# Kernel tuning notes

Measured on AMD Instinct MI355X. Metric: run time of the kernel, lower is better.

Reference implementation:

```python
import jax, jax.numpy as jnp
import numpy as np

N = 100000
IN_C = 128
HID = 8
HEADS = 8
OUT_C = 16
NEG_SLOPE = 0.2  # PyG GATConv default leaky_relu slope
EPS = 1e-16


def setup_inputs() -> dict:
    key = jax.random.key(0)
    ks = jax.random.split(key, 10)
    E = 1600000
    x = jax.random.normal(ks[0], (N, IN_C), dtype=jnp.float32)
    edge_index = jax.random.randint(ks[1], (2, E), 0, N, dtype=jnp.int64)
    g = lambda k, shape: jax.random.normal(k, shape, dtype=jnp.float32) * 0.1
    # layer 1: in -> hid, heads=HEADS, concat
    W1 = g(ks[2], (IN_C, HEADS * HID))
    att_src1 = g(ks[3], (HEADS, HID))
    att_dst1 = g(ks[4], (HEADS, HID))
    b1 = jnp.zeros((HEADS * HID,), jnp.float32)
    # layer 2: hid*heads -> out, heads=1, concat=False (mean)
    W2 = g(ks[5], (HEADS * HID, 1 * OUT_C))
    att_src2 = g(ks[6], (1, OUT_C))
    att_dst2 = g(ks[7], (1, OUT_C))
    b2 = jnp.zeros((OUT_C,), jnp.float32)
    return {"x": x, "edge_index": edge_index, "W1": W1, "att_src1": att_src1,
            "att_dst1": att_dst1, "b1": b1, "W2": W2, "att_src2": att_src2,
            "att_dst2": att_dst2, "b2": b2}


def gat_conv(x, src, dst, W, att_src, att_dst, bias, concat):
    # x: [N, F_in]; src/dst: [E] (self-loops already included)
    H, C = att_src.shape
    h = (x @ W).reshape(N, H, C)                      # [N, H, C]
    a_src = jnp.sum(h * att_src, axis=-1)             # [N, H]
    a_dst = jnp.sum(h * att_dst, axis=-1)             # [N, H]
    alpha = a_src[src] + a_dst[dst]                   # [E, H]
    alpha = jax.nn.leaky_relu(alpha, NEG_SLOPE)
    # segment softmax over incoming edges of each destination node
    amax = jax.ops.segment_max(alpha, dst, num_segments=N)
    alpha = jnp.exp(alpha - amax[dst])
    asum = jax.ops.segment_sum(alpha, dst, num_segments=N)
    alpha = alpha / (asum[dst] + EPS)                 # [E, H]
    # (attention dropout skipped: eval mode)
    out = jax.ops.segment_sum(h[src] * alpha[:, :, None], dst, num_segments=N)  # [N, H, C]
    out = out.reshape(N, H * C) if concat else out.mean(axis=1)
    return out + bias


def reference(x, edge_index, W1, att_src1, att_dst1, b1, W2, att_src2, att_dst2, b2):
    # PyG GATConv adds self-loops by default
    loop = jnp.arange(N, dtype=edge_index.dtype)
    src = jnp.concatenate([edge_index[0], loop])
    dst = jnp.concatenate([edge_index[1], loop])
    h = gat_conv(x, src, dst, W1, att_src1, att_dst1, b1, concat=True)
    h = jax.nn.relu(h)
    out = gat_conv(h, src, dst, W2, att_src2, att_dst2, b2, concat=False)
    return jax.nn.relu(out)
```

## Files before the change

kernel.cpp:

```cpp
#include <hip/hip_runtime.h>
#include <hip/hip_fp16.h>

#define IN_C 128
#define NEG 0.2f
#define GAT_EPS 1e-16f
#define B_N 128
#define NB_MAX 1024
#define TILE 2048
#define GEMM_BLKS 782
#define CAP 2560
#define CS_STRIDE 72

typedef _Float16 half8 __attribute__((ext_vector_type(8)));
typedef float f32x4 __attribute__((ext_vector_type(4)));

static __device__ inline unsigned f2h(float f) {
    _Float16 h = (_Float16)f;
    unsigned short u;
    __builtin_memcpy(&u, &h, 2);
    return (unsigned)u;
}

__global__ __launch_bounds__(256) void k2_kernel(
    const float* __restrict__ x, const float* __restrict__ W1,
    const float* __restrict__ att_s1, const float* __restrict__ att_d1,
    float* __restrict__ hp, __half* __restrict__ a_src1, float* __restrict__ a_dst1,
    const int* __restrict__ ei, int* __restrict__ bucketCnt, unsigned* __restrict__ ebuf,
    int E, int Etot, int NB, int N, int egrid)
{
    __shared__ __align__(16) char smem[26112];
    int tid = threadIdx.x;

    if ((int)blockIdx.x < egrid) {
        int* lcnt  = (int*)smem;
        int* lbase = lcnt + NB_MAX;
        for (int i = tid; i < NB; i += 256) lcnt[i] = 0;
        __syncthreads();
        int base = (int)blockIdx.x * TILE;
        for (int k = tid; k < TILE; k += 256) {
            int e = base + k;
            if (e < Etot) {
                int dst = (e < E) ? ei[E + e] : (e - E);
                atomicAdd(&lcnt[dst >> 7], 1);
            }
        }
        __syncthreads();
        for (int i = tid; i < NB; i += 256) {
            int c = lcnt[i];
            lbase[i] = c ? (i * CAP + atomicAdd(&bucketCnt[i], c)) : 0;
        }
        __syncthreads();
        for (int i = tid; i < NB; i += 256) lcnt[i] = 0;
        __syncthreads();
        for (int k = tid; k < TILE; k += 256) {
            int e = base + k;
            if (e < Etot) {
                int src, dst;
                if (e < E) { src = ei[e]; dst = ei[E + e]; }
                else       { src = dst = e - E; }
                int b = dst >> 7;
                int r = atomicAdd(&lcnt[b], 1);
                int pos = lbase[b] + r;
                if (pos < (b + 1) * CAP)
                    ebuf[pos] = ((unsigned)(dst & (B_N - 1)) << 25) | (unsigned)src;
            }
        }
        return;
    }

    _Float16* bfrag = (_Float16*)smem;
    _Float16* csbase = (_Float16*)(smem + 16384);
    float* attS = (float*)(smem + 16384 + 9216);
    float* attD = attS + 64;
    if (tid < 64) { attS[tid] = att_s1[tid]; attD[tid] = att_d1[tid]; }
    for (int idx = tid; idx < 8192; idx += 256) {
        int f = idx >> 9;
        int l = (idx >> 3) & 63;
        int j = idx & 7;
        int k0 = f >> 2, nt = f & 3;
        int row = k0 * 32 + ((l >> 4) << 3) + j;
        int col = (nt << 4) + (l & 15);
        bfrag[idx] = (_Float16)W1[row * 64 + col];
    }
    __syncthreads();

    int lane = tid & 63, wid = tid >> 6;
    _Float16* csw = csbase + wid * (16 * CS_STRIDE);
    int mrow = lane & 15;
    int kgrp = lane >> 4;
    const half8* bf8 = (const half8*)bfrag;
    int ntiles = (N + 15) >> 4;
    int gb = (int)blockIdx.x - egrid;
    for (int t0 = (gb << 3) + (wid << 1); t0 < ntiles; t0 += (GEMM_BLKS << 3)) {
        bool has1 = (t0 + 1) < ntiles;
        int n0 = t0 << 4;
        int arow0 = n0 + mrow;        if (arow0 >= N) arow0 = N - 1;
        int arow1 = n0 + 16 + mrow;   if (arow1 >= N) arow1 = N - 1;
        const float* xr0 = x + (size_t)arow0 * IN_C + (kgrp << 3);
        const float* xr1 = x + (size_t)arow1 * IN_C + (kgrp << 3);
        f32x4 accs[2][4] = {};
        #pragma unroll
        for (int k0 = 0; k0 < 4; ++k0) {
            float4 xa0 = *(const float4*)(xr0 + k0 * 32);
            float4 xb0 = *(const float4*)(xr0 + k0 * 32 + 4);
            float4 xa1 = *(const float4*)(xr1 + k0 * 32);
            float4 xb1 = *(const float4*)(xr1 + k0 * 32 + 4);
            half8 a0, a1;
            a0[0] = (_Float16)xa0.x; a0[1] = (_Float16)xa0.y;
            a0[2] = (_Float16)xa0.z; a0[3] = (_Float16)xa0.w;
            a0[4] = (_Float16)xb0.x; a0[5] = (_Float16)xb0.y;
            a0[6] = (_Float16)xb0.z; a0[7] = (_Float16)xb0.w;
            a1[0] = (_Float16)xa1.x; a1[1] = (_Float16)xa1.y;
            a1[2] = (_Float16)xa1.z; a1[3] = (_Float16)xa1.w;
            a1[4] = (_Float16)xb1.x; a1[5] = (_Float16)xb1.y;
            a1[6] = (_Float16)xb1.z; a1[7] = (_Float16)xb1.w;
            #pragma unroll
            for (int nt = 0; nt < 4; ++nt) {
                accs[0][nt] = __builtin_amdgcn_mfma_f32_16x16x32_f16(a0, bf8[(k0 * 4 + nt) * 64 + lane], accs[0][nt], 0, 0, 0);
                accs[1][nt] = __builtin_amdgcn_mfma_f32_16x16x32_f16(a1, bf8[(k0 * 4 + nt) * 64 + lane], accs[1][nt], 0, 0, 0);
            }
        }
        #pragma unroll
        for (int tt = 0; tt < 2; ++tt) {
            if (tt == 1 && !has1) break;
            int nb0 = n0 + (tt << 4);
            #pragma unroll
            for (int r = 0; r < 4; ++r) {
                int row = (kgrp << 2) + r;
                csw[row * CS_STRIDE +  0 + mrow] = (_Float16)accs[tt][0][r];
                csw[row * CS_STRIDE + 16 + mrow] = (_Float16)accs[tt][1][r];
                csw[row * CS_STRIDE + 32 + mrow] = (_Float16)accs[tt][2][r];
                csw[row * CS_STRIDE + 48 + mrow] = (_Float16)accs[tt][3][r];
            }
            asm volatile("s_waitcnt lgkmcnt(0)" ::: "memory");
            {
                int node = lane >> 2, cq = lane & 3;
                int n = nb0 + node;
                if (n < N) {
                    const int4* src = (const int4*)(csw + node * CS_STRIDE + (cq << 4));
                    int4 v0 = src[0];
                    int4 v1 = src[1];
                    char* dst = (char*)(hp + (size_t)n * 32) + (cq << 5);
                    ((int4*)dst)[0] = v0;
                    ((int4*)dst)[1] = v1;
                }
            }
            #pragma unroll
            for (int pr = 0; pr < 2; ++pr) {
                int node = (pr << 3) + (lane >> 3), head = lane & 7;
                int n = nb0 + node;
                if (n < N) {
                    const half8* hv = (const half8*)(csw + node * CS_STRIDE + (head << 3));
                    half8 v = *hv;
                    float s = 0.f, d = 0.f;
                    #pragma unroll
                    for (int c = 0; c < 8; ++c) {
                        float vv = (float)v[c];
                        s = fmaf(vv, attS[(head << 3) + c], s);
                        d = fmaf(vv, attD[(head << 3) + c], d);
                    }
                    a_src1[n * 8 + head] = __float2half(s);
                    a_dst1[n * 8 + head] = d;
                }
            }
        }
    }
}

__global__ __launch_bounds__(256) void bucket_sort_kernel(
    const unsigned* __restrict__ ebuf, const int* __restrict__ bucketCnt,
    int2* __restrict__ rowse, int* __restrict__ esrc, int N)
{
    __shared__ int lhist[B_N];
    __shared__ int lstart[B_N];
    __shared__ int wsum1;
    int blk = blockIdx.x, t = threadIdx.x;
    int e0 = blk * CAP;
    int cnt = bucketCnt[blk]; if (cnt > CAP) cnt = CAP;
    int e1 = e0 + cnt;
    if (t < B_N) lhist[t] = 0;
    __syncthreads();
    for (int k = e0 + t; k < e1; k += 256)
        atomicAdd(&lhist[ebuf[k] >> 25], 1);
    __syncthreads();
    int lane = t & 63;
    if (t < B_N) {
        int s = lhist[t];
        for (int off = 1; off < 64; off <<= 1) {
            int u = __shfl_up(s, off);
            if (lane >= off) s += u;
        }
        lstart[t] = s;
        if (t == 63) wsum1 = s;
    }
    __syncthreads();
    if (t < B_N) {
        int s = lstart[t];
        if (t >= 64) s += wsum1;
        int excl = s - lhist[t];
        lstart[t] = excl;
        int n = blk * B_N + t;
        if (n < N) rowse[n] = make_int2(e0 + excl, e0 + excl + lhist[t]);
    }
    __syncthreads();
    if (t < B_N) lhist[t] = 0;
    __syncthreads();
    for (int k = e0 + t; k < e1; k += 256) {
        unsigned pk = ebuf[k];
        int d = pk >> 25;
        int r = atomicAdd(&lhist[d], 1);
        esrc[e0 + lstart[d] + r] = (int)(pk & 0x1FFFFFF);
    }
}

__global__ __launch_bounds__(256) void agg1g2_kernel(
    const int* __restrict__ esrc, const int2* __restrict__ rowse,
    const float* __restrict__ hp, const __half* __restrict__ a_src1,
    const float* __restrict__ a_dst1, const float* __restrict__ b1,
    const float* __restrict__ W2, const float* __restrict__ att_s2,
    const float* __restrict__ att_d2, __half* __restrict__ h2w,
    float* __restrict__ a_src2, float* __restrict__ a_dst2, int N)
{
    __shared__ _Float16 w2frag[1024];
    __shared__ _Float16 h2s[4][16][64];
    __shared__ float cs[4][16 * 20];
    int tid = threadIdx.x;
    for (int idx = tid; idx < 1024; idx += 256) {
        int f = idx >> 9, l = (idx >> 3) & 63, j = idx & 7;
        int row = f * 32 + ((l >> 4) << 3) + j;
        int col = l & 15;
        w2frag[idx] = (_Float16)W2[row * 16 + col];
    }
    __syncthreads();

    int lane = tid & 63, wid = tid >> 6;
    int half = lane >> 5, c2 = lane & 31;
    int h = c2 >> 2;
    int ch = c2 & 7;
    int sbase = half * 32 + h;
    float2 bb = *(const float2*)(b1 + 2 * c2);
    int mrow = lane & 15, kgrp = lane >> 4;
    const half8* w2bf8 = (const half8*)w2frag;
    float* csw = &cs[wid][0];
    int ech = (lane & 3) << 2;
    float as0 = att_s2[ech], as1 = att_s2[ech + 1], as2 = att_s2[ech + 2], as3 = att_s2[ech + 3];
    float ad0 = att_d2[ech], ad1 = att_d2[ech + 1], ad2 = att_d2[ech + 2], ad3 = att_d2[ech + 3];

    int ngroups = (N + 63) >> 6;
    for (int grp = blockIdx.x; grp < ngroups; grp += gridDim.x) {
        int wbase = (grp << 6) + (wid << 4);
        for (int sub = 0; sub < 8; ++sub) {
            int nloc = (sub << 1) + half;
            int n = wbase + nloc;
            bool act = (n < N);
            int nn = act ? n : 0;
            int2 se = rowse[nn];
            int p = se.x;
            int end = act ? se.y : se.x;
            float ad_f = a_dst1[nn * 8 + h];
            float ad_c = a_dst1[nn * 8 + ch];
            float ax = 0.f, ay = 0.f, wsum = 0.f;
            for (; p + 3 < end; p += 4) {
                int s0 = esrc[p], s1 = esrc[p + 1], s2 = esrc[p + 2], s3 = esrc[p + 3];
                int se_ = (c2 & 16) ? ((c2 & 8) ? s3 : s2) : ((c2 & 8) ? s1 : s0);
                float ac = __half2float(a_src1[se_ * 8 + ch]) + ad_c;
                ac = (ac > 0.f) ? ac : NEG * ac;
                float wl = __expf(ac);
                float w0 = __shfl(wl, sbase);
                float w1 = __shfl(wl, sbase + 8);
                float w2 = __shfl(wl, sbase + 16);
                float w3 = __shfl(wl, sbase + 24);
                __half2 q0 = ((const __half2*)(hp + (size_t)s0 * 32))[c2];
                __half2 q1 = ((const __half2*)(hp + (size_t)s1 * 32))[c2];
                __half2 q2 = ((const __half2*)(hp + (size_t)s2 * 32))[c2];
                __half2 q3 = ((const __half2*)(hp + (size_t)s3 * 32))[c2];
                ax = fmaf(w0, __low2float(q0), ax);  ay = fmaf(w0, __high2float(q0), ay);
                ax = fmaf(w1, __low2float(q1), ax);  ay = fmaf(w1, __high2float(q1), ay);
                ax = fmaf(w2, __low2float(q2), ax);  ay = fmaf(w2, __high2float(q2), ay);
                ax = fmaf(w3, __low2float(q3), ax);  ay = fmaf(w3, __high2float(q3), ay);
                wsum += (w0 + w1) + (w2 + w3);
            }
            for (; p < end; ++p) {
                int s0 = esrc[p];
                float a0 = __half2float(a_src1[s0 * 8 + h]) + ad_f;
                __half2 q0 = ((const __half2*)(hp + (size_t)s0 * 32))[c2];
                a0 = (a0 > 0.f) ? a0 : NEG * a0;
                float w0 = __expf(a0);
                ax = fmaf(w0, __low2float(q0), ax);
                ay = fmaf(w0, __high2float(q0), ay);
                wsum += w0;
            }
            float inv = 1.f / (wsum + GAT_EPS);
            float vx = fmaf(ax, inv, bb.x);
            float vy = fmaf(ay, inv, bb.y);
            vx = (act && vx > 0.f) ? vx : 0.f;
            vy = (act && vy > 0.f) ? vy : 0.f;
            ((__half2*)&h2s[wid][nloc][0])[c2] =
                __halves2half2(__float2half(vx), __float2half(vy));
        }
        asm volatile("s_waitcnt lgkmcnt(0)" ::: "memory");
        f32x4 acc = {0, 0, 0, 0};
        const half8* ar = (const half8*)&h2s[wid][mrow][0];
        acc = __builtin_amdgcn_mfma_f32_16x16x32_f16(ar[kgrp], w2bf8[lane], acc, 0, 0, 0);
        acc = __builtin_amdgcn_mfma_f32_16x16x32_f16(ar[4 + kgrp], w2bf8[64 + lane], acc, 0, 0, 0);
        #pragma unroll
        for (int r = 0; r < 4; ++r)
            csw[((kgrp << 2) + r) * 20 + mrow] = acc[r];
        asm volatile("s_waitcnt lgkmcnt(0)" ::: "memory");
        int node = lane >> 2;
        int n = wbase + node;
        if (n < N) {
            float4 v = *(const float4*)&csw[node * 20 + ech];
            unsigned pk0 = f2h(v.x) | (f2h(v.y) << 16);
            unsigned pk1 = f2h(v.z) | (f2h(v.w) << 16);
            *(int2*)((char*)(h2w + (size_t)n * 16) + (ech << 1)) = make_int2((int)pk0, (int)pk1);
            float s = fmaf(v.x, as0, fmaf(v.y, as1, fmaf(v.z, as2, v.w * as3)));
            float d = fmaf(v.x, ad0, fmaf(v.y, ad1, fmaf(v.z, ad2, v.w * ad3)));
            s += __shfl_xor(s, 1); d += __shfl_xor(d, 1);
            s += __shfl_xor(s, 2); d += __shfl_xor(d, 2);
            if ((lane & 3) == 0) { a_src2[n] = s; a_dst2[n] = d; }
        }
    }
}

__global__ __launch_bounds__(256) void agg2_kernel(
    const int* __restrict__ esrc, const int2* __restrict__ rowse,
    const __half* __restrict__ h2w, const float* __restrict__ a_src2,
    const float* __restrict__ a_dst2, const float* __restrict__ b2,
    float* __restrict__ out, int N)
{
    int wslot = (blockIdx.x * 256 + threadIdx.x) >> 6;
    int nw = (gridDim.x * 256) >> 6;
    int lane = threadIdx.x & 63;
    int oct = lane >> 3, c2 = lane & 7;
    for (int base = wslot * 8; base < N; base += nw * 8) {
        int n = base + oct;
        bool act = (n < N);
        int nn = act ? n : 0;
        int2 se = rowse[nn];
        int p = se.x;
        int end = act ? se.y : se.x;
        float ad = a_dst2[nn];
        float ax = 0.f, ay = 0.f, wsum = 0.f;
        for (; p + 3 < end; p += 4) {
            int s0 = esrc[p], s1 = esrc[p + 1], s2 = esrc[p + 2], s3 = esrc[p + 3];
            float a0 = a_src2[s0] + ad;
            float a1 = a_src2[s1] + ad;
            float a2 = a_src2[s2] + ad;
            float a3 = a_src2[s3] + ad;
            __half2 q0 = ((const __half2*)(h2w + (size_t)s0 * 16))[c2];
            __half2 q1 = ((const __half2*)(h2w + (size_t)s1 * 16))[c2];
            __half2 q2 = ((const __half2*)(h2w + (size_t)s2 * 16))[c2];
            __half2 q3 = ((const __half2*)(h2w + (size_t)s3 * 16))[c2];
            a0 = (a0 > 0.f) ? a0 : NEG * a0;
            a1 = (a1 > 0.f) ? a1 : NEG * a1;
            a2 = (a2 > 0.f) ? a2 : NEG * a2;
            a3 = (a3 > 0.f) ? a3 : NEG * a3;
            float w0 = __expf(a0), w1 = __expf(a1), w2 = __expf(a2), w3 = __expf(a3);
            ax = fmaf(w0, __low2float(q0), ax);  ay = fmaf(w0, __high2float(q0), ay);
            ax = fmaf(w1, __low2float(q1), ax);  ay = fmaf(w1, __high2float(q1), ay);
            ax = fmaf(w2, __low2float(q2), ax);  ay = fmaf(w2, __high2float(q2), ay);
            ax = fmaf(w3, __low2float(q3), ax);  ay = fmaf(w3, __high2float(q3), ay);
            wsum += (w0 + w1) + (w2 + w3);
        }
        for (; p < end; ++p) {
            int s0 = esrc[p];
            float a0 = a_src2[s0] + ad;
            __half2 q0 = ((const __half2*)(h2w + (size_t)s0 * 16))[c2];
            a0 = (a0 > 0.f) ? a0 : NEG * a0;
            float w0 = __expf(a0);
            ax = fmaf(w0, __low2float(q0), ax);
            ay = fmaf(w0, __high2float(q0), ay);
            wsum += w0;
        }
        if (act) {
            float inv = 1.f / (wsum + GAT_EPS);
            float2 bb = *(const float2*)(b2 + 2 * c2);
            float2 o;
            o.x = fmaf(ax, inv, bb.x);
            o.y = fmaf(ay, inv, bb.y);
            o.x = o.x > 0.f ? o.x : 0.f;
            o.y = o.y > 0.f ? o.y : 0.f;
            ((float2*)(out + (size_t)n * 16))[c2] = o;
        }
    }
}

extern "C" void kernel_launch(void* const* d_in, const int* in_sizes, int n_in,
                              void* d_out, int out_size, void* d_ws, size_t ws_size,
                              hipStream_t stream)
{
    const float* x      = (const float*)d_in[0];
    const int*   ei     = (const int*)  d_in[1];
    const float* W1     = (const float*)d_in[2];
    const float* att_s1 = (const float*)d_in[3];
    const float* att_d1 = (const float*)d_in[4];
    const float* b1     = (const float*)d_in[5];
    const float* W2     = (const float*)d_in[6];
    const float* att_s2 = (const float*)d_in[7];
    const float* att_d2 = (const float*)d_in[8];
    const float* b2     = (const float*)d_in[9];
    float* out = (float*)d_out;

    int N = in_sizes[0] / IN_C;
    int E = in_sizes[1] / 2;
    int Etot = E + N;
    int NB = (N + B_N - 1) / B_N;

    float* ws = (float*)d_ws;
    float*  hp      = ws;
    __half* a_src1  = (__half*)(hp + (size_t)N * 32);
    float*  a_dst1  = (float*)a_src1 + (size_t)N * 4;
    __half* h2w     = (__half*)(a_dst1 + (size_t)N * 8);
    float*  a_src2  = (float*)h2w + (size_t)N * 8;
    float*  a_dst2  = a_src2 + (size_t)N;
    int2* rowse     = (int2*)(a_dst2 + (size_t)N);
    int* bucketCnt  = (int*)(rowse + N);
    int* esrc       = bucketCnt + NB_MAX;
    unsigned* ebuf  = (unsigned*)(esrc + (size_t)NB * CAP);

    int egrid = (Etot + TILE - 1) / TILE;

    hipMemsetAsync(bucketCnt, 0, NB_MAX * sizeof(int), stream);
    k2_kernel<<<egrid + GEMM_BLKS, 256, 0, stream>>>(
        x, W1, att_s1, att_d1, hp, a_src1, a_dst1, ei, bucketCnt, ebuf,
        E, Etot, NB, N, egrid);
    bucket_sort_kernel<<<NB, 256, 0, stream>>>(ebuf, bucketCnt, rowse, esrc, N);

    {
        int ngroups = (N + 63) >> 6;
        agg1g2_kernel<<<ngroups, 256, 0, stream>>>(
            esrc, rowse, hp, a_src1, a_dst1, b1,
            W2, att_s2, att_d2, h2w, a_src2, a_dst2, N);
    }
    agg2_kernel<<<1024, 256, 0, stream>>>(esrc, rowse, h2w, a_src2, a_dst2, b2, out, N);
}
```

Baseline: 158.2 us.

## Bucket edges into 1024-node superbuckets with 1024-thread sort blocks

Replaces the 128-node destination buckets with 1024-node superbuckets: the scatter phase now keeps only 98 shared counters per block and does far fewer global atomics, with a larger edge tile per block. The second-pass sort uses 1024-thread blocks and a two-level wave scan to build per-node row ranges within each superbucket. This trades many small sort blocks for about 98 large ones, which may underuse the GPU's compute units. Packing 17 bits of source id assumes N below 131072, and a fixed per-superbucket capacity of 20480 assumes balanced degrees.

```diff
diff --git a/kernel.cpp b/kernel.cpp
--- a/kernel.cpp
+++ b/kernel.cpp
@@ -4,11 +4,12 @@
 #define IN_C 128
 #define NEG 0.2f
 #define GAT_EPS 1e-16f
-#define B_N 128
-#define NB_MAX 1024
-#define TILE 2048
+#define NSB_MAX 128
+#define SB_SHIFT 10
+#define SRC_MASK 0x1FFFF
+#define TILE 4096
 #define GEMM_BLKS 782
-#define CAP 2560
+#define CAP_SB 20480
 #define CS_STRIDE 72
 
 typedef _Float16 half8 __attribute__((ext_vector_type(8)));
@@ -25,32 +26,32 @@
     const float* __restrict__ x, const float* __restrict__ W1,
     const float* __restrict__ att_s1, const float* __restrict__ att_d1,
     float* __restrict__ hp, __half* __restrict__ a_src1, float* __restrict__ a_dst1,
-    const int* __restrict__ ei, int* __restrict__ bucketCnt, unsigned* __restrict__ ebuf,
-    int E, int Etot, int NB, int N, int egrid)
+    const int* __restrict__ ei, int* __restrict__ sbCnt, unsigned* __restrict__ ebuf,
+    int E, int Etot, int NSB, int N, int egrid)
 {
     __shared__ __align__(16) char smem[26112];
     int tid = threadIdx.x;
 
     if ((int)blockIdx.x < egrid) {
         int* lcnt  = (int*)smem;
-        int* lbase = lcnt + NB_MAX;
-        for (int i = tid; i < NB; i += 256) lcnt[i] = 0;
+        int* lbase = lcnt + NSB_MAX;
+        for (int i = tid; i < NSB; i += 256) lcnt[i] = 0;
         __syncthreads();
         int base = (int)blockIdx.x * TILE;
         for (int k = tid; k < TILE; k += 256) {
             int e = base + k;
             if (e < Etot) {
                 int dst = (e < E) ? ei[E + e] : (e - E);
-                atomicAdd(&lcnt[dst >> 7], 1);
+                atomicAdd(&lcnt[dst >> SB_SHIFT], 1);
             }
         }
         __syncthreads();
-        for (int i = tid; i < NB; i += 256) {
+        for (int i = tid; i < NSB; i += 256) {
             int c = lcnt[i];
-            lbase[i] = c ? (i * CAP + atomicAdd(&bucketCnt[i], c)) : 0;
+            lbase[i] = c ? (i * CAP_SB + atomicAdd(&sbCnt[i], c)) : 0;
         }
         __syncthreads();
-        for (int i = tid; i < NB; i += 256) lcnt[i] = 0;
+        for (int i = tid; i < NSB; i += 256) lcnt[i] = 0;
         __syncthreads();
         for (int k = tid; k < TILE; k += 256) {
             int e = base + k;
@@ -58,11 +59,11 @@
                 int src, dst;
                 if (e < E) { src = ei[e]; dst = ei[E + e]; }
                 else       { src = dst = e - E; }
-                int b = dst >> 7;
+                int b = dst >> SB_SHIFT;
                 int r = atomicAdd(&lcnt[b], 1);
                 int pos = lbase[b] + r;
-                if (pos < (b + 1) * CAP)
-                    ebuf[pos] = ((unsigned)(dst & (B_N - 1)) << 25) | (unsigned)src;
+                if (pos < (b + 1) * CAP_SB)
+                    ebuf[pos] = ((unsigned)(dst & 1023) << 17) | (unsigned)src;
             }
         }
         return;
@@ -167,49 +168,53 @@
     }
 }
 
-__global__ __launch_bounds__(256) void bucket_sort_kernel(
-    const unsigned* __restrict__ ebuf, const int* __restrict__ bucketCnt,
+__global__ __launch_bounds__(1024) void sb_sort_kernel(
+    const unsigned* __restrict__ ebuf, const int* __restrict__ sbCnt,
     int2* __restrict__ rowse, int* __restrict__ esrc, int N)
 {
-    __shared__ int lhist[B_N];
-    __shared__ int lstart[B_N];
-    __shared__ int wsum1;
+    __shared__ int lhist[1024];
+    __shared__ int lstart[1024];
+    __shared__ int wsums[16];
     int blk = blockIdx.x, t = threadIdx.x;
-    int e0 = blk * CAP;
-    int cnt = bucketCnt[blk]; if (cnt > CAP) cnt = CAP;
+    int e0 = blk * CAP_SB;
+    int cnt = sbCnt[blk]; if (cnt > CAP_SB) cnt = CAP_SB;
     int e1 = e0 + cnt;
-    if (t < B_N) lhist[t] = 0;
-    __syncthreads();
-    for (int k = e0 + t; k < e1; k += 256)
-        atomicAdd(&lhist[ebuf[k] >> 25], 1);
-    __syncthreads();
-    int lane = t & 63;
-    if (t < B_N) {
-        int s = lhist[t];
-        for (int off = 1; off < 64; off <<= 1) {
-            int u = __shfl_up(s, off);
-            if (lane >= off) s += u;
-        }
-        lstart[t] = s;
-        if (t == 63) wsum1 = s;
-    }
-    __syncthreads();
-    if (t < B_N) {
-        int s = lstart[t];
-        if (t >= 64) s += wsum1;
-        int excl = s - lhist[t];
-        lstart[t] = excl;
-        int n = blk * B_N + t;
-        if (n < N) rowse[n] = make_int2(e0 + excl, e0 + excl + lhist[t]);
-    }
-    __syncthreads();
-    if (t < B_N) lhist[t] = 0;
-    __syncthreads();
-    for (int k = e0 + t; k < e1; k += 256) {
+    lhist[t] = 0;
+    __syncthreads();
+    for (int k = e0 + t; k < e1; k += 1024)
+        atomicAdd(&lhist[ebuf[k] >> 17], 1);
+    __syncthreads();
+    int lane = t & 63, wv = t >> 6;
+    int v = lhist[t];
+    int s = v;
+    for (int off = 1; off < 64; off <<= 1) {
+        int u = __shfl_up(s, off);
+        if (lane >= off) s += u;
+    }
+    if (lane == 63) wsums[wv] = s;
+    __syncthreads();
+    if (t < 64) {
+        int ws = (lane < 16) ? wsums[lane] : 0;
+        for (int off = 1; off < 16; off <<= 1) {
+            int u = __shfl_up(ws, off);
+            if (lane >= off) ws += u;
+        }
+        if (lane < 16) wsums[lane] = ws;
+    }
+    __syncthreads();
+    int woff = (wv > 0) ? wsums[wv - 1] : 0;
+    int excl = woff + s - v;
+    lstart[t] = excl;
+    int n = (blk << SB_SHIFT) + t;
+    if (n < N) rowse[n] = make_int2(e0 + excl, e0 + excl + v);
+    __syncthreads();
+    lhist[t] = 0;
+    __syncthreads();
+    for (int k = e0 + t; k < e1; k += 1024) {
         unsigned pk = ebuf[k];
-        int d = pk >> 25;
+        int d = pk >> 17;
         int r = atomicAdd(&lhist[d], 1);
-        esrc[e0 + lstart[d] + r] = (int)(pk & 0x1FFFFFF);
+        esrc[e0 + lstart[d] + r] = (int)(pk & SRC_MASK);
     }
 }
 
@@ -405,7 +410,7 @@
     int N = in_sizes[0] / IN_C;
     int E = in_sizes[1] / 2;
     int Etot = E + N;
-    int NB = (N + B_N - 1) / B_N;
+    int NSB = (N + 1023) >> SB_SHIFT;
 
     float* ws = (float*)d_ws;
     float*  hp      = ws;
@@ -415,17 +420,17 @@
     float*  a_src2  = (float*)h2w + (size_t)N * 8;
     float*  a_dst2  = a_src2 + (size_t)N;
     int2* rowse     = (int2*)(a_dst2 + (size_t)N);
-    int* bucketCnt  = (int*)(rowse + N);
-    int* esrc       = bucketCnt + NB_MAX;
-    unsigned* ebuf  = (unsigned*)(esrc + (size_t)NB * CAP);
+    int* sbCnt      = (int*)(rowse + N);
+    int* esrc       = sbCnt + NSB_MAX;
+    unsigned* ebuf  = (unsigned*)(esrc + (size_t)NSB * CAP_SB);
 
     int egrid = (Etot + TILE - 1) / TILE;
 
-    hipMemsetAsync(bucketCnt, 0, NB_MAX * sizeof(int), stream);
+    hipMemsetAsync(sbCnt, 0, NSB_MAX * sizeof(int), stream);
     k2_kernel<<<egrid + GEMM_BLKS, 256, 0, stream>>>(
-        x, W1, att_s1, att_d1, hp, a_src1, a_dst1, ei, bucketCnt, ebuf,
-        E, Etot, NB, N, egrid);
-    bucket_sort_kernel<<<NB, 256, 0, stream>>>(ebuf, bucketCnt, rowse, esrc, N);
+        x, W1, att_s1, att_d1, hp, a_src1, a_dst1, ei, sbCnt, ebuf,
+        E, Etot, NSB, N, egrid);
+    sb_sort_kernel<<<NSB, 1024, 0, stream>>>(ebuf, sbCnt, rowse, esrc, N);
 
     {
         int ngroups = (N + 63) >> 6;
```

New measurement: 144.6 us. 1.09x faster.
